# Kernel optimization log

Hardware: AMD Instinct MI355X
Metric: run time of the kernel (lower is better)

## Reference

```python
import jax, jax.numpy as jnp
import numpy as np

N_VOXELS = 80000
IN_CHANNELS = 64
NX, NY = 512, 512
BATCH = 4


def setup_inputs() -> dict:
    key = jax.random.key(0)
    kf, kb, kx, ky = jax.random.split(key, 4)
    voxel_features = jax.random.normal(kf, (N_VOXELS, IN_CHANNELS), dtype=jnp.float32)
    b = jax.random.randint(kb, (N_VOXELS, 1), 0, BATCH, dtype=jnp.int32)
    x = jax.random.randint(kx, (N_VOXELS, 1), 0, NX, dtype=jnp.int32)
    y = jax.random.randint(ky, (N_VOXELS, 1), 0, NY, dtype=jnp.int32)
    coords = jnp.concatenate([b, x, y], axis=1)  # [N, 3] = (batch, x, y)
    return {"voxel_features": voxel_features, "coords": coords, "batch_size": BATCH}


def reference(voxel_features, coords, batch_size):
    # Fused scatter: global flat index over (batch, x, y) in one pass.
    nx, ny, c = NX, NY, voxel_features.shape[1]
    flat_idx = (coords[:, 0].astype(jnp.int32) * (nx * ny)
                + coords[:, 1].astype(jnp.int32) * ny
                + coords[:, 2].astype(jnp.int32))  # [N]
    canvas = jnp.zeros((batch_size * nx * ny, c), dtype=voxel_features.dtype)
    canvas = canvas.at[flat_idx].set(voxel_features)  # scatter rows
    # [B*nx*ny, C] -> [B, C, nx, ny]
    canvas = canvas.reshape(batch_size, nx, ny, c)
    return jnp.transpose(canvas, (0, 3, 1, 2))
```

## Files before the change

### kernel.cpp

```cpp
#include <hip/hip_runtime.h>

#define NXD 512
#define NYD 512

__global__ void ppscatter_init_winner(int4* __restrict__ win4, int n_win4) {
    int i = blockIdx.x * blockDim.x + threadIdx.x;
    if (i < n_win4) win4[i] = make_int4(-1, -1, -1, -1);
}

__global__ void ppscatter_vote(const int* __restrict__ coords, int n,
                               int* __restrict__ winner) {
    int v = blockIdx.x * blockDim.x + threadIdx.x;
    if (v >= n) return;
    int b = coords[3 * v + 0];
    int x = coords[3 * v + 1];
    int y = coords[3 * v + 2];
    atomicMax(&winner[b * (NXD * NYD) + x * NYD + y], v);
}

__global__ void ppscatter_gather(const float* __restrict__ feat,
                                 const int* __restrict__ winner,
                                 float4* __restrict__ out4) {
    int i = blockIdx.x * blockDim.x + threadIdx.x;
    int y4 = i & 127;
    int x  = (i >> 7) & 511;
    int c  = (i >> 16) & 63;
    int b  = i >> 22;

    const int4* win4 = (const int4*)winner;
    int4 w = win4[(b << 16) | (x << 7) | y4];

    float4 val = make_float4(0.f, 0.f, 0.f, 0.f);
    if ((w.x & w.y & w.z & w.w) != -1) {
        if (w.x >= 0) val.x = feat[(w.x << 6) + c];
        if (w.y >= 0) val.y = feat[(w.y << 6) + c];
        if (w.z >= 0) val.z = feat[(w.z << 6) + c];
        if (w.w >= 0) val.w = feat[(w.w << 6) + c];
    }
    out4[i] = val;
}

extern "C" void kernel_launch(void* const* d_in, const int* in_sizes, int n_in,
                              void* d_out, int out_size, void* d_ws, size_t ws_size,
                              hipStream_t stream) {
    const float* feat  = (const float*)d_in[0];
    const int* coords  = (const int*)d_in[1];

    int n = in_sizes[1] / 3;
    int* winner = (int*)d_ws;

    const int T = 256;

    int n_win4 = (4 * NXD * NYD) / 4;
    ppscatter_init_winner<<<(n_win4 + T - 1) / T, T, 0, stream>>>((int4*)winner, n_win4);

    ppscatter_vote<<<(n + T - 1) / T, T, 0, stream>>>(coords, n, winner);

    int n_out4 = out_size / 4;
    ppscatter_gather<<<n_out4 / T, T, 0, stream>>>(feat, winner, (float4*)d_out);
}
```

Baseline: 294.5 us.

## Restructure gather so each thread handles four pixels across all channels

The gather kernel now gives each thread one group of four adjacent pixels and loops over all 64 channels, instead of one thread per (channel, pixel-quad). The winner index is read once per thread rather than once per channel. Feature rows are read as contiguous float4 vectors and transposed in registers before being written to the channel-major output. Empty pixel groups take a fast path that writes only zeros. The trade-off is fewer threads, each with a long store loop and more registers, which may reduce the number of stores in flight.

```diff
diff --git a/kernel.cpp b/kernel.cpp
--- a/kernel.cpp
+++ b/kernel.cpp
@@ -2,6 +2,8 @@
 
 #define NXD 512
 #define NYD 512
+#define CD  64
+#define NPIX (NXD * NYD)
 
 __global__ void ppscatter_init_winner(int4* __restrict__ win4, int n_win4) {
     int i = blockIdx.x * blockDim.x + threadIdx.x;
@@ -15,29 +17,34 @@
     int b = coords[3 * v + 0];
     int x = coords[3 * v + 1];
     int y = coords[3 * v + 2];
-    atomicMax(&winner[b * (NXD * NYD) + x * NYD + y], v);
+    atomicMax(&winner[b * NPIX + x * NYD + y], v);
 }
 
-__global__ void ppscatter_gather(const float* __restrict__ feat,
-                                 const int* __restrict__ winner,
+__global__ void ppscatter_gather(const float4* __restrict__ feat4,
+                                 const int4* __restrict__ win4,
                                  float4* __restrict__ out4) {
     int i = blockIdx.x * blockDim.x + threadIdx.x;
-    int y4 = i & 127;
-    int x  = (i >> 7) & 511;
-    int c  = (i >> 16) & 63;
-    int b  = i >> 22;
+    int4 w = win4[i];
+    int base = ((i >> 16) << 22) | (i & 0xFFFF);
 
-    const int4* win4 = (const int4*)winner;
-    int4 w = win4[(b << 16) | (x << 7) | y4];
-
-    float4 val = make_float4(0.f, 0.f, 0.f, 0.f);
-    if ((w.x & w.y & w.z & w.w) != -1) {
-        if (w.x >= 0) val.x = feat[(w.x << 6) + c];
-        if (w.y >= 0) val.y = feat[(w.y << 6) + c];
-        if (w.z >= 0) val.z = feat[(w.z << 6) + c];
-        if (w.w >= 0) val.w = feat[(w.w << 6) + c];
+    if ((w.x & w.y & w.z & w.w) == -1) {
+        const float4 z = make_float4(0.f, 0.f, 0.f, 0.f);
+        #pragma unroll 8
+        for (int c = 0; c < CD; ++c) out4[base + (c << 16)] = z;
+    } else {
+        const float4 z = make_float4(0.f, 0.f, 0.f, 0.f);
+        #pragma unroll 2
+        for (int g = 0; g < CD / 4; ++g) {
+            float4 fx = (w.x >= 0) ? feat4[w.x * 16 + g] : z;
+            float4 fy = (w.y >= 0) ? feat4[w.y * 16 + g] : z;
+            float4 fz = (w.z >= 0) ? feat4[w.z * 16 + g] : z;
+            float4 fw = (w.w >= 0) ? feat4[w.w * 16 + g] : z;
+            out4[base + ((4 * g + 0) << 16)] = make_float4(fx.x, fy.x, fz.x, fw.x);
+            out4[base + ((4 * g + 1) << 16)] = make_float4(fx.y, fy.y, fz.y, fw.y);
+            out4[base + ((4 * g + 2) << 16)] = make_float4(fx.z, fy.z, fz.z, fw.z);
+            out4[base + ((4 * g + 3) << 16)] = make_float4(fx.w, fy.w, fz.w, fw.w);
+        }
     }
-    out4[i] = val;
 }
 
 extern "C" void kernel_launch(void* const* d_in, const int* in_sizes, int n_in,
@@ -50,12 +57,15 @@
     int* winner = (int*)d_ws;
 
     const int T = 256;
+    int B = out_size / (CD * NPIX);
 
-    int n_win4 = (4 * NXD * NYD) / 4;
+    int n_win4 = (B * NPIX) / 4;
     ppscatter_init_winner<<<(n_win4 + T - 1) / T, T, 0, stream>>>((int4*)winner, n_win4);
 
     ppscatter_vote<<<(n + T - 1) / T, T, 0, stream>>>(coords, n, winner);
 
-    int n_out4 = out_size / 4;
-    ppscatter_gather<<<n_out4 / T, T, 0, stream>>>(feat, winner, (float4*)d_out);
+    int n_groups = (B * NPIX) / 4;
+    ppscatter_gather<<<n_groups / T, T, 0, stream>>>((const float4*)feat,
+                                                     (const int4*)winner,
+                                                     (float4*)d_out);
 }
```

Measured after the change: 430.8 us. +46.2%, slower.
